# Kernel tuning notes

Measured on AMD Instinct MI355X. Metric: run time of the kernel, lower is better.

## Reference

```python
import jax, jax.numpy as jnp
import numpy as np

N_NODES = 100000
N_RELS = 8
N_EDGES = 150000
D_IN = 128
D_OUT = 128


def setup_inputs() -> dict:
    key = jax.random.key(0)
    k1, k2, k3, k4, k5 = jax.random.split(key, 5)
    scale = 1.0 / np.sqrt(D_IN)
    return {
        "x": jax.random.normal(k1, (N_NODES, D_IN), dtype=jnp.float32),
        "weight": jax.random.normal(k2, (N_RELS, D_IN, D_OUT), dtype=jnp.float32) * scale,
        "self_loop_weight": jax.random.normal(k3, (D_IN, D_OUT), dtype=jnp.float32) * scale,
        "bias": jnp.zeros((D_OUT,), dtype=jnp.float32),
        "src": jax.random.randint(k4, (N_RELS, N_EDGES), 0, N_NODES, dtype=jnp.int64),
        "dst": jax.random.randint(k5, (N_RELS, N_EDGES), 0, N_NODES, dtype=jnp.int64),
    }


def reference(x, weight, self_loop_weight, bias, src, dst):
    # Per-relation GraphConv(norm='right'): for each dst node, mean of incoming
    # src features (sum / in-degree, degree clamped to 1), then matmul W_r.
    # HeteroGraphConv sums relation outputs; then self-loop, bias, relu.
    n = x.shape[0]

    def per_rel(s, d, W):
        msgs = jax.ops.segment_sum(x[s], d, num_segments=n)          # [N, D_IN]
        deg = jax.ops.segment_sum(jnp.ones_like(s, dtype=x.dtype), d,
                                  num_segments=n)                     # [N]
        msgs = msgs / jnp.maximum(deg, 1.0)[:, None]
        return msgs @ W                                               # [N, D_OUT]

    agg = jax.vmap(per_rel)(src, dst, weight).sum(axis=0)             # [N, D_OUT]
    out = agg + x @ self_loop_weight + bias
    return jax.nn.relu(out)
```

## Files before the change

### kernel.cpp

```cpp
#include <hip/hip_runtime.h>
#include <hip/hip_bf16.h>
#include <stdint.h>

#define N_NODES 100000
#define N_RELS  8
#define N_EDGES 150000
#define KCOLS   1152
#define CAP     64

#define EB_BLOCKS   587
#define EDGE_SECT   (EB_BLOCKS * N_RELS)
#define CAST_BLOCKS 6250
#define PREP_BLOCKS 576

typedef short bf16x8 __attribute__((ext_vector_type(8)));
typedef float f32x4  __attribute__((ext_vector_type(4)));
typedef unsigned int u32;

__device__ __forceinline__ unsigned short f2b(float f) {
    union { float f; unsigned u; } v; v.f = f;
    unsigned r = v.u + 0x7FFF + ((v.u >> 16) & 1);
    return (unsigned short)(r >> 16);
}

__device__ __forceinline__ void gld16(const void* g, void* lds_uniform) {
    __builtin_amdgcn_global_load_lds(
        (const __attribute__((address_space(1))) u32*)g,
        (__attribute__((address_space(3))) u32*)lds_uniform,
        16, 0, 0);
}


__global__ __launch_bounds__(256) void fused_pre(
    const float* __restrict__ x, const float* __restrict__ W,
    const float* __restrict__ Wself,
    const int* __restrict__ src, const int* __restrict__ dst,
    unsigned short* __restrict__ xb, unsigned short* __restrict__ BT,
    int* __restrict__ cnt, int* __restrict__ ebuf) {
    int b = blockIdx.x;
    if (b < EDGE_SECT) {
        int r = b / EB_BLOCKS, eb = b - r * EB_BLOCKS;
        int e = eb * 256 + threadIdx.x;
        if (e >= N_EDGES) return;
        int s = src[r * N_EDGES + e];
        int d = dst[r * N_EDGES + e];
        int slot = atomicAdd(&cnt[d], 1);
        if (slot < CAP) ebuf[d * CAP + slot] = (r << 17) | s;
    } else if (b < EDGE_SECT + CAST_BLOCKS) {
        int t = (b - EDGE_SECT) * 256 + threadIdx.x;
        if (t >= N_NODES * 16) return;
        int row = t >> 4, g = t & 15;
        const float4* p = (const float4*)(x + (size_t)row * 128 + g * 8);
        float4 a = p[0], bb = p[1];
        unsigned short o[8] = { f2b(a.x), f2b(a.y), f2b(a.z), f2b(a.w),
                                f2b(bb.x), f2b(bb.y), f2b(bb.z), f2b(bb.w) };
        int g2 = (g & 8) | ((g & 7) ^ (row & 7));
        *(int4*)(xb + (size_t)row * 128 + (g2 << 3)) = *(const int4*)o;
    } else {
        int flat = (b - EDGE_SECT - CAST_BLOCKS) * 256 + threadIdx.x;
        if (flat >= 128 * KCOLS) return;
        int n = flat / KCOLS, k = flat - n * KCOLS;
        float v;
        if (k < 1024) {
            int r = k >> 7, kk = k & 127;
            v = W[(r << 14) + (kk << 7) + n];
        } else {
            v = Wself[((k - 1024) << 7) + n];
        }
        int ks = (k & ~63) | ((k & 63) ^ ((n & 7) << 3));
        BT[(size_t)n * KCOLS + ks] = f2b(v);
    }
}

__global__ __launch_bounds__(256) void agg_x(
    const unsigned short* __restrict__ xb, const int* __restrict__ ebuf,
    const int* __restrict__ cnt, unsigned short* __restrict__ Agg) {
    int d = (blockIdx.x << 2) + (threadIdx.x >> 6);
    if (d >= N_NODES) return;
    d = __builtin_amdgcn_readfirstlane(d);
    int lane = threadIdx.x & 63;

    int k = cnt[d]; if (k > CAP) k = CAP;
    k = __builtin_amdgcn_readfirstlane(k);
    int rec = (lane < k) ? ebuf[d * CAP + lane] : -1;
    int rl = rec >> 17;

    const unsigned int* xw = (const unsigned int*)xb;

    unsigned long long mask[8];
#pragma unroll
    for (int r = 0; r < 8; ++r) mask[r] = __ballot(rl == r);

    unsigned long long below = (lane == 63) ? 0x7FFFFFFFFFFFFFFFull
                                            : ((1ull << lane) - 1);
    int pre = 0;
    unsigned long long mymask = 0;
#pragma unroll
    for (int r = 0; r < 8; ++r) {
        pre += (rl > r) ? (int)__popcll(mask[r]) : 0;
        mymask = (rl == r) ? mask[r] : mymask;
    }
    int pos = (rl >= 0) ? (pre + (int)__popcll(mymask & below)) : lane;
    int srt = __builtin_amdgcn_ds_permute(pos << 2, rec);

    int swu = lane ^ ((d & 7) << 2);
    unsigned int* aggRow = (unsigned int*)(Agg + (size_t)d * 1024);

    auto store_r = [&](int rconst, float ax, float ay, int dg) {
        float inv = 1.0f / (float)(dg < 1 ? 1 : dg);
        unsigned int pk = (unsigned int)f2b(ax * inv)
                        | ((unsigned int)f2b(ay * inv) << 16);
        aggRow[(rconst << 6) + swu] = pk;
    };
    auto flush = [&](int r, float ax, float ay) {
        switch (r) {
            case 0: store_r(0, ax, ay, (int)__popcll(mask[0])); break;
            case 1: store_r(1, ax, ay, (int)__popcll(mask[1])); break;
            case 2: store_r(2, ax, ay, (int)__popcll(mask[2])); break;
            case 3: store_r(3, ax, ay, (int)__popcll(mask[3])); break;
            case 4: store_r(4, ax, ay, (int)__popcll(mask[4])); break;
            case 5: store_r(5, ax, ay, (int)__popcll(mask[5])); break;
            case 6: store_r(6, ax, ay, (int)__popcll(mask[6])); break;
            default: store_r(7, ax, ay, (int)__popcll(mask[7])); break;
        }
    };

    float axc = 0.f, ayc = 0.f;
    int cur = 0;
    if (k > 0) cur = __builtin_amdgcn_readlane(srt, 0) >> 17;

    for (int i = 0; i < k; i += 4) {
        int rc4[4];
#pragma unroll
        for (int j = 0; j < 4; ++j) {
            int ii = i + j; if (ii > k - 1) ii = k - 1;
            rc4[j] = __builtin_amdgcn_readlane(srt, ii);
        }
        unsigned int y4[4];
#pragma unroll
        for (int j = 0; j < 4; ++j) {
            int s = rc4[j] & 0x1FFFF;
            y4[j] = xw[(size_t)s * 64 + (lane ^ ((s & 7) << 2))];
        }
#pragma unroll
        for (int j = 0; j < 4; ++j) {
            if (i + j < k) {
                int rr = rc4[j] >> 17;
                if (rr != cur) {
                    flush(cur, axc, ayc);
                    axc = 0.f; ayc = 0.f; cur = rr;
                }
                union { unsigned u; float f; } vx, vy;
                vx.u = y4[j] << 16;
                vy.u = y4[j] & 0xFFFF0000u;
                axc += vx.f;
                ayc += vy.f;
            }
        }
    }
    if (k > 0) flush(cur, axc, ayc);

#pragma unroll
    for (int r = 0; r < 8; ++r)
        if (mask[r] == 0) aggRow[(r << 6) + swu] = 0u;
}

__global__ __launch_bounds__(256) void gemm_out(
    const unsigned short* __restrict__ Agg, const unsigned short* __restrict__ xb,
    const unsigned short* __restrict__ BT, const float* __restrict__ bias,
    float* __restrict__ out) {
    __shared__ short As[2][128 * 64];
    __shared__ short Bs[2][128 * 64];
    int t = threadIdx.x;
    int rowBase = blockIdx.x * 128;

    int w = t >> 6, lane = t & 63;
    int wr = w >> 1, wc = w & 1;
    int ml = lane & 15, quad = lane >> 4;
    int sa = (lane & 7) << 4;

    int ri = lane >> 3;
    int cb = (lane & 7) << 4;

    f32x4 acc[4][4];
#pragma unroll
    for (int i = 0; i < 4; ++i)
#pragma unroll
        for (int j = 0; j < 4; ++j)
            acc[i][j] = (f32x4){0.f, 0.f, 0.f, 0.f};

    auto stage = [&](int buf, int t2) {
        int kc = t2 >> 1, h = t2 & 1;
#pragma unroll
        for (int j = 0; j < 4; ++j) {
            int i = (w << 2) + j;
            int row = (i << 3) + ri;
            int grow = rowBase + row;
            if (grow > N_NODES - 1) grow = N_NODES - 1;
            const char* ga = (kc < 8)
                ? (const char*)Agg + (size_t)grow * 2048 + (kc << 8) + (h << 7) + cb
                : (const char*)xb  + (size_t)grow * 256  + (h << 7) + cb;
            gld16(ga, (char*)&As[buf][0] + (i << 10));
            const char* gb = (const char*)BT + (size_t)row * 2304 + (t2 << 7) + cb;
            gld16(gb, (char*)&Bs[buf][0] + (i << 10));
        }
    };

    auto compute = [&](int buf) {
#pragma unroll
        for (int kb = 0; kb < 2; ++kb) {
            int off = ((kb << 6) + (quad << 4)) ^ sa;
            bf16x8 a[4], b[4];
#pragma unroll
            for (int i = 0; i < 4; ++i)
                a[i] = *(const bf16x8*)((const char*)&As[buf][0] +
                        (((wr << 6) + (i << 4) + ml) << 7) + off);
#pragma unroll
            for (int j = 0; j < 4; ++j)
                b[j] = *(const bf16x8*)((const char*)&Bs[buf][0] +
                        (((wc << 6) + (j << 4) + ml) << 7) + off);
#pragma unroll
            for (int i = 0; i < 4; ++i)
#pragma unroll
                for (int j = 0; j < 4; ++j)
                    acc[i][j] = __builtin_amdgcn_mfma_f32_16x16x32_bf16(a[i], b[j], acc[i][j], 0, 0, 0);
        }
    };

    stage(0, 0);
    asm volatile("s_waitcnt vmcnt(0)" ::: "memory");
    __syncthreads();
    int cur = 0;
    for (int t2 = 0; t2 < 18; ++t2) {
        if (t2 + 1 < 18) stage(cur ^ 1, t2 + 1);
        compute(cur);
        asm volatile("s_waitcnt vmcnt(0)" ::: "memory");
        __syncthreads();
        cur ^= 1;
    }

#pragma unroll
    for (int i = 0; i < 4; ++i) {
#pragma unroll
        for (int j = 0; j < 4; ++j) {
            int col = wc * 64 + j * 16 + ml;
            float bv = bias[col];
#pragma unroll
            for (int rr = 0; rr < 4; ++rr) {
                int row = rowBase + wr * 64 + i * 16 + quad * 4 + rr;
                if (row < N_NODES) {
                    float v = acc[i][j][rr] + bv;
                    out[(size_t)row * 128 + col] = fmaxf(v, 0.f);
                }
            }
        }
    }
}

extern "C" void kernel_launch(void* const* d_in, const int* in_sizes, int n_in,
                              void* d_out, int out_size, void* d_ws, size_t ws_size,
                              hipStream_t stream) {
    const float* x     = (const float*)d_in[0];
    const float* W     = (const float*)d_in[1];
    const float* Wself = (const float*)d_in[2];
    const float* bias  = (const float*)d_in[3];
    const int*   src   = (const int*)d_in[4];
    const int*   dst   = (const int*)d_in[5];
    float* out = (float*)d_out;

    char* ws = (char*)d_ws;
    size_t off = 0;
    unsigned short* Agg = (unsigned short*)(ws + off); off += (size_t)N_NODES * 1024 * 2;
    unsigned short* xb  = (unsigned short*)(ws + off); off += (size_t)N_NODES * 128 * 2;
    unsigned short* BT  = (unsigned short*)(ws + off); off += (size_t)128 * KCOLS * 2;
    int* cnt  = (int*)(ws + off); off += (size_t)N_NODES * 4;
    int* ebuf = (int*)(ws + off); off += (size_t)N_NODES * CAP * 4;

    hipMemsetAsync(cnt, 0, (size_t)N_NODES * 4, stream);

    fused_pre<<<EDGE_SECT + CAST_BLOCKS + PREP_BLOCKS, 256, 0, stream>>>(
        x, W, Wself, src, dst, xb, BT, cnt, ebuf);

    agg_x<<<(N_NODES + 3) / 4, 256, 0, stream>>>(xb, ebuf, cnt, Agg);

    gemm_out<<<(N_NODES + 127) / 128, 256, 0, stream>>>(Agg, xb, BT, bias, out);
}
```

Baseline: 329.0 us.

## Merge memset, preprocessing and aggregation into one cooperative persistent kernel

Replaces the memset, the fused preprocessing kernel and the aggregation kernel with a single cooperative kernel. It uses grid-wide syncs between the counter clear, the edge bucketing/cast/weight transpose phase, and the aggregation phase. Preprocessing work units are visited in a scrambled order to spread the edge-atomic blocks across the grid. The aim is to remove launch gaps and tail effects between stages. In exchange, phases are separated by grid barriers, and the persistent grid may have lower occupancy than independent launches. A fallback path keeps the old launches if the cooperative launch fails.

```diff
diff --git a/kernel.cpp b/kernel.cpp
--- a/kernel.cpp
+++ b/kernel.cpp
@@ -1,6 +1,9 @@
 #include <hip/hip_runtime.h>
 #include <hip/hip_bf16.h>
+#include <hip/hip_cooperative_groups.h>
 #include <stdint.h>
+
+namespace cg = cooperative_groups;
 
 #define N_NODES 100000
 #define N_RELS  8
@@ -12,6 +15,7 @@
 #define EDGE_SECT   (EB_BLOCKS * N_RELS)
 #define CAST_BLOCKS 6250
 #define PREP_BLOCKS 576
+#define TOTAL_PRE   (EDGE_SECT + CAST_BLOCKS + PREP_BLOCKS)
 
 typedef short bf16x8 __attribute__((ext_vector_type(8)));
 typedef float f32x4  __attribute__((ext_vector_type(4)));
@@ -31,54 +35,55 @@
 }
 
 
-__global__ __launch_bounds__(256) void fused_pre(
+__device__ __forceinline__ void pre_unit(
+    unsigned b, int tid,
     const float* __restrict__ x, const float* __restrict__ W,
     const float* __restrict__ Wself,
     const int* __restrict__ src, const int* __restrict__ dst,
     unsigned short* __restrict__ xb, unsigned short* __restrict__ BT,
     int* __restrict__ cnt, int* __restrict__ ebuf) {
-    int b = blockIdx.x;
     if (b < EDGE_SECT) {
         int r = b / EB_BLOCKS, eb = b - r * EB_BLOCKS;
-        int e = eb * 256 + threadIdx.x;
-        if (e >= N_EDGES) return;
-        int s = src[r * N_EDGES + e];
-        int d = dst[r * N_EDGES + e];
-        int slot = atomicAdd(&cnt[d], 1);
-        if (slot < CAP) ebuf[d * CAP + slot] = (r << 17) | s;
+        int e = eb * 256 + tid;
+        if (e < N_EDGES) {
+            int s = src[r * N_EDGES + e];
+            int d = dst[r * N_EDGES + e];
+            int slot = atomicAdd(&cnt[d], 1);
+            if (slot < CAP) ebuf[d * CAP + slot] = (r << 17) | s;
+        }
     } else if (b < EDGE_SECT + CAST_BLOCKS) {
-        int t = (b - EDGE_SECT) * 256 + threadIdx.x;
-        if (t >= N_NODES * 16) return;
-        int row = t >> 4, g = t & 15;
-        const float4* p = (const float4*)(x + (size_t)row * 128 + g * 8);
-        float4 a = p[0], bb = p[1];
-        unsigned short o[8] = { f2b(a.x), f2b(a.y), f2b(a.z), f2b(a.w),
-                                f2b(bb.x), f2b(bb.y), f2b(bb.z), f2b(bb.w) };
-        int g2 = (g & 8) | ((g & 7) ^ (row & 7));
-        *(int4*)(xb + (size_t)row * 128 + (g2 << 3)) = *(const int4*)o;
+        int t = (b - EDGE_SECT) * 256 + tid;
+        if (t < N_NODES * 16) {
+            int row = t >> 4, g = t & 15;
+            const float4* p = (const float4*)(x + (size_t)row * 128 + g * 8);
+            float4 a = p[0], bb = p[1];
+            unsigned short o[8] = { f2b(a.x), f2b(a.y), f2b(a.z), f2b(a.w),
+                                    f2b(bb.x), f2b(bb.y), f2b(bb.z), f2b(bb.w) };
+            int g2 = (g & 8) | ((g & 7) ^ (row & 7));
+            *(int4*)(xb + (size_t)row * 128 + (g2 << 3)) = *(const int4*)o;
+        }
     } else {
-        int flat = (b - EDGE_SECT - CAST_BLOCKS) * 256 + threadIdx.x;
-        if (flat >= 128 * KCOLS) return;
-        int n = flat / KCOLS, k = flat - n * KCOLS;
-        float v;
-        if (k < 1024) {
-            int r = k >> 7, kk = k & 127;
-            v = W[(r << 14) + (kk << 7) + n];
-        } else {
-            v = Wself[((k - 1024) << 7) + n];
-        }
-        int ks = (k & ~63) | ((k & 63) ^ ((n & 7) << 3));
-        BT[(size_t)n * KCOLS + ks] = f2b(v);
-    }
-}
-
-__global__ __launch_bounds__(256) void agg_x(
+        int flat = (int)(b - EDGE_SECT - CAST_BLOCKS) * 256 + tid;
+        if (flat < 128 * KCOLS) {
+            int n = flat / KCOLS, k = flat - n * KCOLS;
+            float v;
+            if (k < 1024) {
+                int r = k >> 7, kk = k & 127;
+                v = W[(r << 14) + (kk << 7) + n];
+            } else {
+                v = Wself[((k - 1024) << 7) + n];
+            }
+            int ks = (k & ~63) | ((k & 63) ^ ((n & 7) << 3));
+            BT[(size_t)n * KCOLS + ks] = f2b(v);
+        }
+    }
+}
+
+__device__ __forceinline__ void agg_one(
+    int d, int lane,
     const unsigned short* __restrict__ xb, const int* __restrict__ ebuf,
     const int* __restrict__ cnt, unsigned short* __restrict__ Agg) {
-    int d = (blockIdx.x << 2) + (threadIdx.x >> 6);
-    if (d >= N_NODES) return;
     d = __builtin_amdgcn_readfirstlane(d);
-    int lane = threadIdx.x & 63;
 
     int k = cnt[d]; if (k > CAP) k = CAP;
     k = __builtin_amdgcn_readfirstlane(k);
@@ -165,6 +170,52 @@
         if (mask[r] == 0) aggRow[(r << 6) + swu] = 0u;
 }
 
+__global__ __launch_bounds__(256, 8) void coop_front(
+    const float* __restrict__ x, const float* __restrict__ W,
+    const float* __restrict__ Wself,
+    const int* __restrict__ src, const int* __restrict__ dst,
+    unsigned short* __restrict__ xb, unsigned short* __restrict__ BT,
+    int* __restrict__ cnt, int* __restrict__ ebuf,
+    unsigned short* __restrict__ Agg) {
+    cg::grid_group g = cg::this_grid();
+
+    for (int i = blockIdx.x * 256 + threadIdx.x; i < N_NODES;
+         i += gridDim.x * 256)
+        cnt[i] = 0;
+    __threadfence();
+    g.sync();
+
+    for (unsigned bu = blockIdx.x; bu < TOTAL_PRE; bu += gridDim.x) {
+        unsigned b = (bu * 7919u) % (unsigned)TOTAL_PRE;
+        pre_unit(b, threadIdx.x, x, W, Wself, src, dst, xb, BT, cnt, ebuf);
+    }
+    __threadfence();
+    g.sync();
+
+    int lane = threadIdx.x & 63;
+    for (int vb = blockIdx.x; vb < (N_NODES + 3) / 4; vb += gridDim.x) {
+        int d = (vb << 2) + (threadIdx.x >> 6);
+        if (d < N_NODES) agg_one(d, lane, xb, ebuf, cnt, Agg);
+    }
+}
+
+__global__ __launch_bounds__(256) void fused_pre(
+    const float* __restrict__ x, const float* __restrict__ W,
+    const float* __restrict__ Wself,
+    const int* __restrict__ src, const int* __restrict__ dst,
+    unsigned short* __restrict__ xb, unsigned short* __restrict__ BT,
+    int* __restrict__ cnt, int* __restrict__ ebuf) {
+    pre_unit(blockIdx.x, threadIdx.x, x, W, Wself, src, dst, xb, BT, cnt, ebuf);
+}
+
+__global__ __launch_bounds__(256) void agg_x(
+    const unsigned short* __restrict__ xb, const int* __restrict__ ebuf,
+    const int* __restrict__ cnt, unsigned short* __restrict__ Agg) {
+    int d = (blockIdx.x << 2) + (threadIdx.x >> 6);
+    if (d >= N_NODES) return;
+    agg_one(d, threadIdx.x & 63, xb, ebuf, cnt, Agg);
+}
+
 __global__ __launch_bounds__(256) void gemm_out(
     const unsigned short* __restrict__ Agg, const unsigned short* __restrict__ xb,
     const unsigned short* __restrict__ BT, const float* __restrict__ bias,
@@ -276,12 +327,26 @@
     int* cnt  = (int*)(ws + off); off += (size_t)N_NODES * 4;
     int* ebuf = (int*)(ws + off); off += (size_t)N_NODES * CAP * 4;
 
-    hipMemsetAsync(cnt, 0, (size_t)N_NODES * 4, stream);
-
-    fused_pre<<<EDGE_SECT + CAST_BLOCKS + PREP_BLOCKS, 256, 0, stream>>>(
-        x, W, Wself, src, dst, xb, BT, cnt, ebuf);
-
-    agg_x<<<(N_NODES + 3) / 4, 256, 0, stream>>>(xb, ebuf, cnt, Agg);
+    int nb = 0;
+    hipError_t qerr = hipOccupancyMaxActiveBlocksPerMultiprocessor(
+        &nb, coop_front, 256, 0);
+    if (qerr != hipSuccess || nb < 1) nb = 1;
+    if (nb > 8) nb = 8;
+    int cgrid = nb * 256;
+    if (cgrid > 2048) cgrid = 2048;
+
+    void* args[] = { (void*)&x, (void*)&W, (void*)&Wself, (void*)&src,
+                     (void*)&dst, (void*)&xb, (void*)&BT, (void*)&cnt,
+                     (void*)&ebuf, (void*)&Agg };
+    hipError_t lerr = hipLaunchCooperativeKernel(
+        (void*)coop_front, dim3(cgrid), dim3(256), args, 0, stream);
+
+    if (lerr != hipSuccess) {
+        hipMemsetAsync(cnt, 0, (size_t)N_NODES * 4, stream);
+        fused_pre<<<TOTAL_PRE, 256, 0, stream>>>(x, W, Wself, src, dst,
+                                                 xb, BT, cnt, ebuf);
+        agg_x<<<(N_NODES + 3) / 4, 256, 0, stream>>>(xb, ebuf, cnt, Agg);
+    }
 
     gemm_out<<<(N_NODES + 127) / 128, 256, 0, stream>>>(Agg, xb, BT, bias, out);
 }
```

Result: slower. 920.6 us (+179.8%).

## Pre-pack weights in MFMA fragment order and load B directly from global

Applied to the files above, without the earlier changes.

The weight prep kernel now writes the transposed bf16 weights in the exact per-lane MFMA fragment order. The GEMM then loads B fragments straight from global memory (served by L2/L1) instead of staging them through LDS, which halves shared memory per block. Launch bounds now request 4 blocks per CU. The B tile is shared by all blocks, so it should stay cache-resident, but each wave's compute step now depends on global-load latency instead of LDS latency.

```diff
diff --git a/kernel.cpp b/kernel.cpp
--- a/kernel.cpp
+++ b/kernel.cpp
@@ -12,6 +12,7 @@
 #define EDGE_SECT   (EB_BLOCKS * N_RELS)
 #define CAST_BLOCKS 6250
 #define PREP_BLOCKS 576
+#define TOTAL_PRE   (EDGE_SECT + CAST_BLOCKS + PREP_BLOCKS)
 
 typedef short bf16x8 __attribute__((ext_vector_type(8)));
 typedef float f32x4  __attribute__((ext_vector_type(4)));
@@ -35,40 +36,47 @@
     const float* __restrict__ x, const float* __restrict__ W,
     const float* __restrict__ Wself,
     const int* __restrict__ src, const int* __restrict__ dst,
-    unsigned short* __restrict__ xb, unsigned short* __restrict__ BT,
+    unsigned short* __restrict__ xb, unsigned short* __restrict__ BT2,
     int* __restrict__ cnt, int* __restrict__ ebuf) {
     int b = blockIdx.x;
+    int tid = threadIdx.x;
     if (b < EDGE_SECT) {
         int r = b / EB_BLOCKS, eb = b - r * EB_BLOCKS;
-        int e = eb * 256 + threadIdx.x;
-        if (e >= N_EDGES) return;
-        int s = src[r * N_EDGES + e];
-        int d = dst[r * N_EDGES + e];
-        int slot = atomicAdd(&cnt[d], 1);
-        if (slot < CAP) ebuf[d * CAP + slot] = (r << 17) | s;
+        int e = eb * 256 + tid;
+        if (e < N_EDGES) {
+            int s = src[r * N_EDGES + e];
+            int d = dst[r * N_EDGES + e];
+            int slot = atomicAdd(&cnt[d], 1);
+            if (slot < CAP) ebuf[d * CAP + slot] = (r << 17) | s;
+        }
     } else if (b < EDGE_SECT + CAST_BLOCKS) {
-        int t = (b - EDGE_SECT) * 256 + threadIdx.x;
-        if (t >= N_NODES * 16) return;
-        int row = t >> 4, g = t & 15;
-        const float4* p = (const float4*)(x + (size_t)row * 128 + g * 8);
-        float4 a = p[0], bb = p[1];
-        unsigned short o[8] = { f2b(a.x), f2b(a.y), f2b(a.z), f2b(a.w),
-                                f2b(bb.x), f2b(bb.y), f2b(bb.z), f2b(bb.w) };
-        int g2 = (g & 8) | ((g & 7) ^ (row & 7));
-        *(int4*)(xb + (size_t)row * 128 + (g2 << 3)) = *(const int4*)o;
+        int t = (b - EDGE_SECT) * 256 + tid;
+        if (t < N_NODES * 16) {
+            int row = t >> 4, g = t & 15;
+            const float4* p = (const float4*)(x + (size_t)row * 128 + g * 8);
+            float4 a = p[0], bb = p[1];
+            unsigned short o[8] = { f2b(a.x), f2b(a.y), f2b(a.z), f2b(a.w),
+                                    f2b(bb.x), f2b(bb.y), f2b(bb.z), f2b(bb.w) };
+            int g2 = (g & 8) | ((g & 7) ^ (row & 7));
+            *(int4*)(xb + (size_t)row * 128 + (g2 << 3)) = *(const int4*)o;
+        }
     } else {
-        int flat = (b - EDGE_SECT - CAST_BLOCKS) * 256 + threadIdx.x;
-        if (flat >= 128 * KCOLS) return;
-        int n = flat / KCOLS, k = flat - n * KCOLS;
-        float v;
-        if (k < 1024) {
-            int r = k >> 7, kk = k & 127;
-            v = W[(r << 14) + (kk << 7) + n];
-        } else {
-            v = Wself[((k - 1024) << 7) + n];
-        }
-        int ks = (k & ~63) | ((k & 63) ^ ((n & 7) << 3));
-        BT[(size_t)n * KCOLS + ks] = f2b(v);
+        int flat = (b - EDGE_SECT - CAST_BLOCKS) * 256 + tid;
+        if (flat < 128 * KCOLS) {
+            int n = flat / KCOLS, k = flat - n * KCOLS;
+            float v;
+            if (k < 1024) {
+                int r = k >> 7, kk = k & 127;
+                v = W[(r << 14) + (kk << 7) + n];
+            } else {
+                v = Wself[((k - 1024) << 7) + n];
+            }
+            int t2 = k >> 6, kb = (k >> 5) & 1, quad = (k >> 3) & 3, e = k & 7;
+            int wc = n >> 6, j = (n >> 4) & 3, ml = n & 15;
+            size_t idx = ((((((size_t)t2 * 2 + kb) * 2 + wc) * 4 + j) * 4 + quad)
+                          << 7) + (ml << 3) + e;
+            BT2[idx] = f2b(v);
+        }
     }
 }
 
@@ -165,12 +173,11 @@
         if (mask[r] == 0) aggRow[(r << 6) + swu] = 0u;
 }
 
-__global__ __launch_bounds__(256) void gemm_out(
+__global__ __launch_bounds__(256, 4) void gemm_out(
     const unsigned short* __restrict__ Agg, const unsigned short* __restrict__ xb,
-    const unsigned short* __restrict__ BT, const float* __restrict__ bias,
+    const unsigned short* __restrict__ BT2, const float* __restrict__ bias,
     float* __restrict__ out) {
     __shared__ short As[2][128 * 64];
-    __shared__ short Bs[2][128 * 64];
     int t = threadIdx.x;
     int rowBase = blockIdx.x * 128;
 
@@ -201,12 +208,10 @@
                 ? (const char*)Agg + (size_t)grow * 2048 + (kc << 8) + (h << 7) + cb
                 : (const char*)xb  + (size_t)grow * 256  + (h << 7) + cb;
             gld16(ga, (char*)&As[buf][0] + (i << 10));
-            const char* gb = (const char*)BT + (size_t)row * 2304 + (t2 << 7) + cb;
-            gld16(gb, (char*)&Bs[buf][0] + (i << 10));
-        }
-    };
-
-    auto compute = [&](int buf) {
+        }
+    };
+
+    auto compute = [&](int buf, int t2) {
 #pragma unroll
         for (int kb = 0; kb < 2; ++kb) {
             int off = ((kb << 6) + (quad << 4)) ^ sa;
@@ -216,9 +221,11 @@
                 a[i] = *(const bf16x8*)((const char*)&As[buf][0] +
                         (((wr << 6) + (i << 4) + ml) << 7) + off);
 #pragma unroll
-            for (int j = 0; j < 4; ++j)
-                b[j] = *(const bf16x8*)((const char*)&Bs[buf][0] +
-                        (((wc << 6) + (j << 4) + ml) << 7) + off);
+            for (int j = 0; j < 4; ++j) {
+                size_t fb = (((((size_t)(t2 << 1) + kb) * 2 + wc) * 4 + j) << 9)
+                          + ((size_t)lane << 3);
+                b[j] = *(const bf16x8*)&BT2[fb];
+            }
 #pragma unroll
             for (int i = 0; i < 4; ++i)
 #pragma unroll
@@ -233,7 +240,7 @@
     int cur = 0;
     for (int t2 = 0; t2 < 18; ++t2) {
         if (t2 + 1 < 18) stage(cur ^ 1, t2 + 1);
-        compute(cur);
+        compute(cur, t2);
         asm volatile("s_waitcnt vmcnt(0)" ::: "memory");
         __syncthreads();
         cur ^= 1;
@@ -272,16 +279,16 @@
     size_t off = 0;
     unsigned short* Agg = (unsigned short*)(ws + off); off += (size_t)N_NODES * 1024 * 2;
     unsigned short* xb  = (unsigned short*)(ws + off); off += (size_t)N_NODES * 128 * 2;
-    unsigned short* BT  = (unsigned short*)(ws + off); off += (size_t)128 * KCOLS * 2;
+    unsigned short* BT2 = (unsigned short*)(ws + off); off += (size_t)128 * KCOLS * 2;
     int* cnt  = (int*)(ws + off); off += (size_t)N_NODES * 4;
     int* ebuf = (int*)(ws + off); off += (size_t)N_NODES * CAP * 4;
 
     hipMemsetAsync(cnt, 0, (size_t)N_NODES * 4, stream);
 
-    fused_pre<<<EDGE_SECT + CAST_BLOCKS + PREP_BLOCKS, 256, 0, stream>>>(
-        x, W, Wself, src, dst, xb, BT, cnt, ebuf);
+    fused_pre<<<TOTAL_PRE, 256, 0, stream>>>(x, W, Wself, src, dst,
+                                             xb, BT2, cnt, ebuf);
 
     agg_x<<<(N_NODES + 3) / 4, 256, 0, stream>>>(xb, ebuf, cnt, Agg);
 
-    gemm_out<<<(N_NODES + 127) / 128, 256, 0, stream>>>(Agg, xb, BT, bias, out);
-}
+    gemm_out<<<(N_NODES + 127) / 128, 256, 0, stream>>>(Agg, xb, BT2, bias, out);
+}
```

After: 319.9 us, median of 2. -2.8%, faster.
